# Performance work log

Measured on AMD Instinct MI355X. Metric: run time of the kernel, lower is better.

Reference implementation:

```python
import jax, jax.numpy as jnp
import numpy as np

NH = 12
LEVEL = 4  # Lmin = 2**LEVEL = 16


def _build_sets(T, Lmin):
    l_list, r_list = [], []
    L = Lmin
    while L <= T:
        for i in range(T // L):
            l_list.append(i * L)
            r_list.append((i + 1) * L - 1)
        L *= 2
    return np.asarray(l_list, np.int32), np.asarray(r_list, np.int32)


def _get_slice(x_cum, l_idx, r_idx):
    # x_cum: [B,nh,T,hs]; returns inclusive range-sums x[l..r] via cumsum diffs
    r = x_cum[:, :, r_idx, :]
    l = x_cum[:, :, np.maximum(np.asarray(l_idx) - 1, 0), :]
    mask = (np.asarray(l_idx) >= 1).astype(x_cum.dtype)[None, None, :, None]
    return r - l * mask


def _get_slice_dyn(x_cum, l_idx, r_idx):
    # same but with traced/jnp indices (tail term)
    r = x_cum[:, :, r_idx, :]
    l = x_cum[:, :, jnp.maximum(l_idx - 1, 0), :]
    mask = (l_idx >= 1).astype(x_cum.dtype)[None, None, :, None]
    return r - l * mask


def setup_inputs() -> dict:
    key = jax.random.key(0)
    k0, k1, k2, k3 = jax.random.split(key, 4)
    B, T, C = 8, 2048, 768
    hs = C // NH
    s = 0.02
    return {
        "x": jax.random.normal(k0, (B, T, C), jnp.float32),
        "Wqkv": jax.random.normal(k1, (3 * C, C), jnp.float32) * s,
        "Wproj": jax.random.normal(k2, (C, C), jnp.float32) * s,
        "Wv": jax.random.normal(k3, (hs, hs * hs), jnp.float32) * s,
        "bv": jnp.zeros((hs,), jnp.float32),
    }


def reference(x, Wqkv, Wproj, Wv, bv):
    B, T, C = x.shape
    nh = NH
    hs = C // nh
    Lmin = 2 ** LEVEL
    scale = 1.0 / jnp.sqrt(jnp.asarray(hs, x.dtype))

    qkv = x @ Wqkv.T  # [B,T,3C]
    q, k, v0 = jnp.split(qkv, 3, axis=-1)
    q = q.reshape(B, T, nh, hs).transpose(0, 2, 1, 3)   # [B,nh,T,hs]
    k = k.reshape(B, T, nh, hs).transpose(0, 2, 1, 3)
    v0 = v0.reshape(B, T, nh, hs).transpose(0, 2, 1, 3)

    # v = v_proj(outer(k, v0).flatten)  == einsum with Wv reshaped [hs,hs,hs]
    Wv3 = Wv.reshape(hs, hs, hs)
    v = jnp.einsum('bhti,bhtj,eij->bhte', k, v0, Wv3) + bv

    k_cum = jnp.cumsum(k, axis=2)
    v_cum = jnp.cumsum(v, axis=2)

    l_idx, r_idx = _build_sets(T, Lmin)  # static dyadic sets
    K = _get_slice(k_cum, l_idx, r_idx)  # [B,nh,S,hs]
    V = _get_slice(v_cum, l_idx, r_idx)

    t_idx = jnp.arange(T)
    mask = t_idx[:, None] >= jnp.asarray(r_idx)[None, :]  # [T,S]
    logits = jnp.einsum('bhtd,bhsd->bhts', q, K) * scale
    logits = jnp.where(mask[None, None], logits, -jnp.inf)

    # tail: remainder within the current Lmin block
    l_tail = (t_idx // Lmin) * Lmin
    K_tail = _get_slice_dyn(k_cum, l_tail, t_idx)  # [B,nh,T,hs]
    V_tail = _get_slice_dyn(v_cum, l_tail, t_idx)
    tail_logits = jnp.sum(q * K_tail, axis=-1) * scale  # [B,nh,T]

    att = jax.nn.softmax(jnp.concatenate([logits, tail_logits[..., None]], axis=-1), axis=-1)
    out = jnp.einsum('bhts,bhsd->bhtd', att[..., :-1], V) + att[..., -1:] * V_tail
    out = out.transpose(0, 2, 1, 3).reshape(B, T, C)
    return out @ Wproj.T
```

## Files before the change

kernel.cpp:

```cpp
#include <hip/hip_runtime.h>


typedef float  f32x4  __attribute__((ext_vector_type(4)));
typedef _Float16 half8 __attribute__((ext_vector_type(8)));
typedef _Float16 half4 __attribute__((ext_vector_type(4)));

#define DEV __device__ __forceinline__
#define MFMA16(a, b, c) __builtin_amdgcn_mfma_f32_16x16x32_f16((a), (b), (c), 0, 0, 0)
#define GLOAD16(gp, lp)                                                  \
  __builtin_amdgcn_global_load_lds(                                      \
      (const __attribute__((address_space(1))) unsigned int*)(gp),       \
      (__attribute__((address_space(3))) unsigned int*)(lp), 16, 0, 0)

__global__ __launch_bounds__(256) void k_cast16(const float* __restrict__ in,
                                                _Float16* __restrict__ outh, int n4) {
  int i = blockIdx.x * 256 + threadIdx.x;
  if (i >= n4) return;
  f32x4 v = ((const f32x4*)in)[i];
  half4 o;
#pragma unroll
  for (int c = 0; c < 4; ++c) o[c] = (_Float16)v[c];
  ((half4*)outh)[i] = o;
}

__global__ __launch_bounds__(256, 3) void k_gemm_qkv(
    const _Float16* __restrict__ A16, const _Float16* __restrict__ B16,
    _Float16* __restrict__ qo, _Float16* __restrict__ ko, _Float16* __restrict__ v0o) {
  __shared__ _Float16 sA[128][64], sB[128][64];
  const int K = 768;
  int tid = threadIdx.x, lane = tid & 63, wave = tid >> 6;
  int l15 = lane & 15, g = lane >> 4;
  int wr = wave >> 1, wc = wave & 1;
  int wg = (blockIdx.x & 7) * 288 + (blockIdx.x >> 3);
  int n0 = (wg % 18) * 128, m0 = (wg / 18) * 128;
  f32x4 acc[4][4];
#pragma unroll
  for (int a = 0; a < 4; ++a)
#pragma unroll
    for (int b = 0; b < 4; ++b) acc[a][b] = f32x4{0.f, 0.f, 0.f, 0.f};
  int rsel = lane >> 3;
  int csel = (lane & 7) ^ rsel;
  for (int k0 = 0; k0 < K; k0 += 64) {
#pragma unroll
    for (int r = 0; r < 4; ++r) {
      int row = wave * 32 + r * 8 + rsel;
      GLOAD16(&A16[(size_t)(m0 + row) * K + k0 + csel * 8], &sA[wave * 32 + r * 8][0]);
      GLOAD16(&B16[(size_t)(n0 + row) * K + k0 + csel * 8], &sB[wave * 32 + r * 8][0]);
    }
    __syncthreads();
#pragma unroll
    for (int kk = 0; kk < 2; ++kk) {
      int kc = kk * 4 + g;
      int cc = ((kc ^ (l15 & 7)) << 3);
      half8 af[4], bf[4];
#pragma unroll
      for (int mf = 0; mf < 4; ++mf) af[mf] = *(const half8*)&sA[wr * 64 + mf * 16 + l15][cc];
#pragma unroll
      for (int nf = 0; nf < 4; ++nf) bf[nf] = *(const half8*)&sB[wc * 64 + nf * 16 + l15][cc];
#pragma unroll
      for (int mf = 0; mf < 4; ++mf)
#pragma unroll
        for (int nf = 0; nf < 4; ++nf)
          acc[mf][nf] = MFMA16(af[mf], bf[nf], acc[mf][nf]);
    }
    __syncthreads();
  }
  int sec = n0 / 768;
  int nb = n0 - sec * 768;
#pragma unroll
  for (int mf = 0; mf < 4; ++mf)
#pragma unroll
    for (int nf = 0; nf < 4; ++nf)
#pragma unroll
      for (int r = 0; r < 4; ++r) {
        int m = m0 + wr * 64 + mf * 16 + (g << 2) + r;
        int n = nb + wc * 64 + nf * 16 + l15;
        int b = m >> 11, t = m & 2047;
        int h = n >> 6, d = n & 63;
        size_t idx = (((size_t)b * 12 + h) * 2048 + t) * 64 + d;
        _Float16 val = (_Float16)acc[mf][nf][r];
        if (sec == 0) qo[idx] = val;
        else if (sec == 1) ko[idx] = val;
        else v0o[idx] = val;
      }
}

__global__ __launch_bounds__(256, 3) void k_veins(
    const _Float16* __restrict__ kh, const _Float16* __restrict__ v0g,
    const _Float16* __restrict__ Wvh, const float* __restrict__ bv,
    _Float16* __restrict__ vout) {
  __shared__ _Float16 ks[256][72];
  __shared__ _Float16 sB[2][64][64];
  int tid = threadIdx.x, lane = tid & 63, wave = tid >> 6;
  int l15 = lane & 15, g = lane >> 4, g8 = g << 3;
  size_t row0 = (size_t)blockIdx.x * 256;

  int srow_lo = wave * 8 + (lane >> 3);
  int scsrc = (lane & 7) ^ (lane >> 3);
  auto STAGE = [&](int b, int i) {
#pragma unroll
    for (int h = 0; h < 2; ++h) {
      GLOAD16(&Wvh[(size_t)(h * 32 + srow_lo) * 4096 + i * 64 + (scsrc << 3)],
              ((_Float16*)sB) + (size_t)b * 4096 + (h * 256 + wave * 64) * 8);
    }
  };

#pragma unroll
  for (int r = 0; r < 8; ++r) {
    int row = (tid >> 3) + r * 32;
    int c8 = (tid & 7) << 3;
    *(half8*)&ks[row][c8] = *(const half8*)&kh[(row0 + row) * 64 + c8];
  }
  half8 v0r[4][2];
#pragma unroll
  for (int mf = 0; mf < 4; ++mf) {
    size_t rb = (row0 + wave * 64 + mf * 16 + l15) * 64;
#pragma unroll
    for (int kk = 0; kk < 2; ++kk)
      v0r[mf][kk] = *(const half8*)&v0g[rb + kk * 32 + g8];
  }
  f32x4 acc[4][4];
#pragma unroll
  for (int a = 0; a < 4; ++a)
#pragma unroll
    for (int b = 0; b < 4; ++b) acc[a][b] = f32x4{0.f, 0.f, 0.f, 0.f};

  STAGE(0, 0);
  __syncthreads();
  int r0 = wave * 64 + l15;
  for (int i8 = 0; i8 < 8; ++i8) {
    half8 kr0 = *(const half8*)&ks[r0][i8 * 8];
    half8 kr1 = *(const half8*)&ks[r0 + 16][i8 * 8];
    half8 kr2 = *(const half8*)&ks[r0 + 32][i8 * 8];
    half8 kr3 = *(const half8*)&ks[r0 + 48][i8 * 8];
#pragma unroll
    for (int ii = 0; ii < 8; ++ii) {
      int i = i8 * 8 + ii;
      int cur = i & 1;
      if (i < 63) STAGE(cur ^ 1, i + 1);
      half8 b0[4], b1[4];
#pragma unroll
      for (int nf = 0; nf < 4; ++nf) {
        b0[nf] = *(const half8*)&sB[cur][nf * 16 + l15][((g ^ (l15 & 7)) << 3)];
        b1[nf] = *(const half8*)&sB[cur][nf * 16 + l15][(((4 + g) ^ (l15 & 7)) << 3)];
      }
      _Float16 kv0 = kr0[ii], kv1 = kr1[ii], kv2 = kr2[ii], kv3 = kr3[ii];
      {
        half8 a0 = v0r[0][0] * kv0, a1 = v0r[1][0] * kv1;
        half8 a2 = v0r[2][0] * kv2, a3 = v0r[3][0] * kv3;
#pragma unroll
        for (int nf = 0; nf < 4; ++nf) {
          acc[0][nf] = MFMA16(a0, b0[nf], acc[0][nf]);
          acc[1][nf] = MFMA16(a1, b0[nf], acc[1][nf]);
          acc[2][nf] = MFMA16(a2, b0[nf], acc[2][nf]);
          acc[3][nf] = MFMA16(a3, b0[nf], acc[3][nf]);
        }
      }
      {
        half8 a0 = v0r[0][1] * kv0, a1 = v0r[1][1] * kv1;
        half8 a2 = v0r[2][1] * kv2, a3 = v0r[3][1] * kv3;
#pragma unroll
        for (int nf = 0; nf < 4; ++nf) {
          acc[0][nf] = MFMA16(a0, b1[nf], acc[0][nf]);
          acc[1][nf] = MFMA16(a1, b1[nf], acc[1][nf]);
          acc[2][nf] = MFMA16(a2, b1[nf], acc[2][nf]);
          acc[3][nf] = MFMA16(a3, b1[nf], acc[3][nf]);
        }
      }
      __syncthreads();
    }
  }
#pragma unroll
  for (int mf = 0; mf < 4; ++mf)
#pragma unroll
    for (int nf = 0; nf < 4; ++nf) {
      int e = (nf << 4) + l15;
      float bve = bv[e];
#pragma unroll
      for (int r = 0; r < 4; ++r) {
        int row = wave * 64 + mf * 16 + (g << 2) + r;
        vout[(row0 + row) * 64 + e] = (_Float16)(acc[mf][nf][r] + bve);
      }
    }
}

__global__ __launch_bounds__(256) void k_segments(
    const _Float16* __restrict__ kmat, const _Float16* __restrict__ vmat,
    _Float16* __restrict__ Ks, _Float16* __restrict__ Vt) {
  __shared__ float Ls[255][64];
  int bh = blockIdx.x, tid = threadIdx.x;
  size_t bh2048 = (size_t)bh * 2048;
  for (int task = tid; task < 8192; task += 256) {
    int seg = task >> 6, d = task & 63;
    const _Float16* p = kmat + (bh2048 + seg * 16) * 64 + d;
    float s = 0.f;
#pragma unroll
    for (int u = 0; u < 16; ++u) s += (float)p[u * 64];
    Ls[seg][d] = s;
  }
  __syncthreads();
  {
    int bprev = 0, bcur = 128, cnt = 64;
    for (int lev = 1; lev < 8; ++lev) {
      for (int task = tid; task < cnt * 64; task += 256) {
        int i = task >> 6, d = task & 63;
        Ls[bcur + i][d] = Ls[bprev + 2 * i][d] + Ls[bprev + 2 * i + 1][d];
      }
      __syncthreads();
      bprev = bcur; bcur += cnt; cnt >>= 1;
    }
  }
  for (int task = tid; task < 16384; task += 256) {
    int seg = task >> 6;
    float v = (seg < 255) ? Ls[seg][task & 63] : 0.f;
    Ks[(size_t)bh * 16384 + task] = (_Float16)v;
  }
  __syncthreads();
  for (int task = tid; task < 8192; task += 256) {
    int seg = task >> 6, d = task & 63;
    const _Float16* p = vmat + (bh2048 + seg * 16) * 64 + d;
    float s = 0.f;
#pragma unroll
    for (int u = 0; u < 16; ++u) s += (float)p[u * 64];
    Ls[seg][d] = s;
  }
  __syncthreads();
  {
    int bprev = 0, bcur = 128, cnt = 64;
    for (int lev = 1; lev < 8; ++lev) {
      for (int task = tid; task < cnt * 64; task += 256) {
        int i = task >> 6, d = task & 63;
        Ls[bcur + i][d] = Ls[bprev + 2 * i][d] + Ls[bprev + 2 * i + 1][d];
      }
      __syncthreads();
      bprev = bcur; bcur += cnt; cnt >>= 1;
    }
  }
  for (int task = tid; task < 16384; task += 256) {
    int d = task >> 8, seg = task & 255;
    float v = (seg < 255) ? Ls[seg][d] : 0.f;
    Vt[(size_t)bh * 16384 + task] = (_Float16)v;
  }
}

__global__ __launch_bounds__(256) void k_tails(
    const _Float16* __restrict__ km, const _Float16* __restrict__ vm,
    _Float16* __restrict__ tKg, _Float16* __restrict__ tVt) {
  int bh = blockIdx.x >> 3, seg16 = (blockIdx.x & 7) * 16;
  int wave = threadIdx.x >> 6, lane = threadIdx.x & 63;
  for (int task = wave; task < 32; task += 4) {
    int blk = seg16 + (task >> 1);
    size_t base = ((size_t)bh * 2048 + blk * 16) * 64 + lane;
    if (!(task & 1)) {
      float ka = 0.f;
      _Float16* o = tKg + (((size_t)bh * 128 + blk) * 16) * 64 + lane;
#pragma unroll
      for (int t = 0; t < 16; ++t) {
        ka += (float)km[base + t * 64];
        o[t * 64] = (_Float16)ka;
      }
    } else {
      float va = 0.f;
      half8 lo = {}, hi = {};
#pragma unroll
      for (int t = 0; t < 8; ++t) {
        va += (float)vm[base + t * 64];
        lo[t] = (_Float16)va;
      }
#pragma unroll
      for (int t = 0; t < 8; ++t) {
        va += (float)vm[base + (t + 8) * 64];
        hi[t] = (_Float16)va;
      }
      _Float16* o = tVt + (((size_t)bh * 128 + blk) * 64 + lane) * 16;
      ((half8*)o)[0] = lo;
      ((half8*)o)[1] = hi;
    }
  }
}

__global__ __launch_bounds__(256, 3) void k_attn2(
    const _Float16* __restrict__ qm,
    const _Float16* __restrict__ tKg, const _Float16* __restrict__ tVt,
    const _Float16* __restrict__ Ks, const _Float16* __restrict__ Vt,
    _Float16* __restrict__ outp) {
  __shared__ __align__(16) _Float16 P[4][16][280];
  int tid = threadIdx.x, lane = tid & 63, wave = tid >> 6;
  int orig = blockIdx.y * 32 + blockIdx.x;
  int wg = (orig & 7) * 384 + (orig >> 3);
  int tile = wg & 31, bh = wg >> 5;
  int t0 = tile * 64, tw0 = t0 + wave * 16;
  int blkw = tile * 4 + wave;
  size_t bh2048 = (size_t)bh * 2048;
  int l15 = lane & 15, g = lane >> 4, g8 = g << 3;

  half8 qf0, qf1;
  {
    const _Float16* qp = qm + (bh2048 + tw0 + l15) * 64 + g8;
    qf0 = *(const half8*)qp;
    qf1 = *(const half8*)(qp + 32);
  }
  half8 t0f, t1f;
  {
    const _Float16* tp = tKg + (((size_t)bh * 128 + blkw) * 16 + l15) * 64 + g8;
    t0f = *(const half8*)tp;
    t1f = *(const half8*)(tp + 32);
  }
  unsigned mA = 0, mE = 0;
#pragma unroll
  for (int nf = 0; nf < 16; ++nf) {
    int seg = nf * 16 + l15;
    if (seg < 255) {
      int m = 256 - seg;
      int cl = 32 - __clz(m - 1);
      int lev = 8 - cl;
      int rdx = (seg - (256 - (256 >> lev)) + 1) * (16 << lev) - 1;
      if (rdx < tw0) mA |= 1u << nf;
      else if (rdx == tw0 + 15) mE |= 1u << nf;
    }
  }

  const _Float16* KsB = Ks + (size_t)bh * 16384;
  const _Float16* VB = Vt + (size_t)bh * 16384;
  f32x4 acc[17];
#pragma unroll
  for (int i = 0; i < 17; ++i) acc[i] = f32x4{0.f, 0.f, 0.f, 0.f};

#define LOADKS(dst, ks_)                                                 \
  {                                                                      \
    const _Float16* ph = KsB + (size_t)((ks_) * 32 + l15) * 64 + g8;     \
    (dst)[0] = *(const half8*)ph;                                        \
    (dst)[1] = *(const half8*)(ph + 32);                                 \
    (dst)[2] = *(const half8*)(ph + 1024);                               \
    (dst)[3] = *(const half8*)(ph + 1056);                               \
  }
#define QKMFMA(src, ks_)                                                 \
  {                                                                      \
    acc[2 * (ks_)]     = MFMA16(qf0, (src)[0], acc[2 * (ks_)]);          \
    acc[2 * (ks_)]     = MFMA16(qf1, (src)[1], acc[2 * (ks_)]);          \
    acc[2 * (ks_) + 1] = MFMA16(qf0, (src)[2], acc[2 * (ks_) + 1]);      \
    acc[2 * (ks_) + 1] = MFMA16(qf1, (src)[3], acc[2 * (ks_) + 1]);      \
  }

  half8 fr[3][4];
  LOADKS(fr[0], 0);
  LOADKS(fr[1], 1);
  __builtin_amdgcn_s_setprio(1);
#pragma unroll
  for (int ks = 0; ks < 8; ++ks) {
    if (ks < 6) LOADKS(fr[(ks + 2) % 3], ks + 2);
    QKMFMA(fr[ks % 3], ks);
  }
  acc[16] = MFMA16(qf0, t0f, acc[16]);
  acc[16] = MFMA16(qf1, t1f, acc[16]);
  __builtin_amdgcn_s_setprio(0);

  const float c = 0.125f * 1.44269504f;
  float mx[4], sm[4], et[4];
#pragma unroll
  for (int r = 0; r < 4; ++r) {
    int tr = g * 4 + r;
    mx[r] = (l15 == tr) ? acc[16][r] * c : -3.0e38f;
  }
#pragma unroll
  for (int nf = 0; nf < 16; ++nf) {
    bool bA = (mA >> nf) & 1, bE = (mE >> nf) & 1;
#pragma unroll
    for (int r = 0; r < 4; ++r) {
      bool u = bA || (bE && g == 3 && r == 3);
      if (u) mx[r] = fmaxf(mx[r], acc[nf][r] * c);
    }
  }
#pragma unroll
  for (int off = 1; off < 16; off <<= 1)
#pragma unroll
    for (int r = 0; r < 4; ++r) mx[r] = fmaxf(mx[r], __shfl_xor(mx[r], off));
#pragma unroll
  for (int r = 0; r < 4; ++r) {
    int tr = g * 4 + r;
    et[r] = (l15 == tr) ? exp2f(acc[16][r] * c - mx[r]) : 0.f;
    sm[r] = et[r];
  }
#pragma unroll
  for (int nf = 0; nf < 16; ++nf) {
    bool bA = (mA >> nf) & 1, bE = (mE >> nf) & 1;
#pragma unroll
    for (int r = 0; r < 4; ++r) {
      bool u = bA || (bE && g == 3 && r == 3);
      float e = u ? exp2f(acc[nf][r] * c - mx[r]) : 0.f;
      acc[nf][r] = e;
      sm[r] += e;
    }
  }
#pragma unroll
  for (int off = 1; off < 16; off <<= 1)
#pragma unroll
    for (int r = 0; r < 4; ++r) sm[r] += __shfl_xor(sm[r], off);
  float inv[4];
#pragma unroll
  for (int r = 0; r < 4; ++r) inv[r] = 1.f / sm[r];

#define LOADVT(dst, ks_)                                                 \
  {                                                                      \
    const _Float16* pv = VB + (size_t)l15 * 256 + (ks_) * 32 + g8;       \
    (dst)[0] = *(const half8*)pv;                                        \
    (dst)[1] = *(const half8*)(pv + 16 * 256);                           \
    (dst)[2] = *(const half8*)(pv + 32 * 256);                           \
    (dst)[3] = *(const half8*)(pv + 48 * 256);                           \
  }

  half8 vr[3][4];
  LOADVT(vr[0], 0);
  LOADVT(vr[1], 1);

  {
    half4 z4 = {};
    *(half4*)&P[wave][lane >> 2][256 + (lane & 3) * 4] = z4;
  }
#pragma unroll
  for (int nf = 0; nf < 16; ++nf)
#pragma unroll
    for (int r = 0; r < 4; ++r)
      P[wave][g * 4 + r][nf * 16 + l15] = (_Float16)acc[nf][r];
#pragma unroll
  for (int r = 0; r < 4; ++r)
    if (l15 == g * 4 + r) P[wave][l15][256 + l15] = (_Float16)et[r];

  f32x4 oa[4];
#pragma unroll
  for (int i = 0; i < 4; ++i) oa[i] = f32x4{0.f, 0.f, 0.f, 0.f};
  __builtin_amdgcn_s_setprio(1);
#pragma unroll
  for (int ks = 0; ks < 8; ++ks) {
    if (ks < 6) LOADVT(vr[(ks + 2) % 3], ks + 2);
    half8 pa = *(const half8*)&P[wave][l15][ks * 32 + g8];
#pragma unroll
    for (int n2 = 0; n2 < 4; ++n2)
      oa[n2] = MFMA16(pa, vr[ks % 3][n2], oa[n2]);
  }
  {
    half8 pa = *(const half8*)&P[wave][l15][256 + (g & 1) * 8];
    const _Float16* tvb = tVt + ((size_t)bh * 128 + blkw) * 1024;
#pragma unroll
    for (int n2 = 0; n2 < 4; ++n2) {
      half8 vt = {};
      if (g < 2)
        vt = *(const half8*)(tvb + (size_t)(n2 * 16 + l15) * 16 + g8);
      oa[n2] = MFMA16(pa, vt, oa[n2]);
    }
  }
  __builtin_amdgcn_s_setprio(0);
#undef LOADKS
#undef QKMFMA
#undef LOADVT
  int b = bh / 12, h = bh - b * 12;
  size_t obase = ((size_t)b * 2048 + tw0) * 768 + h * 64;
#pragma unroll
  for (int n2 = 0; n2 < 4; ++n2)
#pragma unroll
    for (int r = 0; r < 4; ++r)
      outp[obase + (size_t)(g * 4 + r) * 768 + n2 * 16 + l15] = (_Float16)(oa[n2][r] * inv[r]);
}

__global__ __launch_bounds__(256, 3) void k_gemm_proj(
    const _Float16* __restrict__ A16, const _Float16* __restrict__ B16,
    float* __restrict__ C) {
  __shared__ _Float16 sA[128][64], sB[128][64];
  const int K = 768;
  int tid = threadIdx.x, lane = tid & 63, wave = tid >> 6;
  int l15 = lane & 15, g = lane >> 4;
  int wr = wave >> 1, wc = wave & 1;
  int wg = (blockIdx.x & 7) * 96 + (blockIdx.x >> 3);
  int n0 = (wg % 6) * 128, m0 = (wg / 6) * 128;
  f32x4 acc[4][4];
#pragma unroll
  for (int a = 0; a < 4; ++a)
#pragma unroll
    for (int b = 0; b < 4; ++b) acc[a][b] = f32x4{0.f, 0.f, 0.f, 0.f};
  int rsel = lane >> 3;
  int csel = (lane & 7) ^ rsel;
  for (int k0 = 0; k0 < K; k0 += 64) {
#pragma unroll
    for (int r = 0; r < 4; ++r) {
      int row = wave * 32 + r * 8 + rsel;
      GLOAD16(&A16[(size_t)(m0 + row) * K + k0 + csel * 8], &sA[wave * 32 + r * 8][0]);
      GLOAD16(&B16[(size_t)(n0 + row) * K + k0 + csel * 8], &sB[wave * 32 + r * 8][0]);
    }
    __syncthreads();
#pragma unroll
    for (int kk = 0; kk < 2; ++kk) {
      int kc = kk * 4 + g;
      int cc = ((kc ^ (l15 & 7)) << 3);
      half8 af[4], bf[4];
#pragma unroll
      for (int mf = 0; mf < 4; ++mf) af[mf] = *(const half8*)&sA[wr * 64 + mf * 16 + l15][cc];
#pragma unroll
      for (int nf = 0; nf < 4; ++nf) bf[nf] = *(const half8*)&sB[wc * 64 + nf * 16 + l15][cc];
#pragma unroll
      for (int mf = 0; mf < 4; ++mf)
#pragma unroll
        for (int nf = 0; nf < 4; ++nf)
          acc[mf][nf] = MFMA16(af[mf], bf[nf], acc[mf][nf]);
    }
    __syncthreads();
  }
#pragma unroll
  for (int mf = 0; mf < 4; ++mf)
#pragma unroll
    for (int nf = 0; nf < 4; ++nf)
#pragma unroll
      for (int r = 0; r < 4; ++r) {
        int m = m0 + wr * 64 + mf * 16 + (g << 2) + r;
        int n = n0 + wc * 64 + nf * 16 + l15;
        C[(size_t)m * 768 + n] = acc[mf][nf][r];
      }
}

extern "C" void kernel_launch(void* const* d_in, const int* in_sizes, int n_in,
                              void* d_out, int out_size, void* d_ws, size_t ws_size,
                              hipStream_t stream) {
  const float* x = (const float*)d_in[0];
  const float* Wqkv = (const float*)d_in[1];
  const float* Wproj = (const float*)d_in[2];
  const float* Wv = (const float*)d_in[3];
  const float* bv = (const float*)d_in[4];
  float* out = (float*)d_out;
  char* ws = (char*)d_ws;
  size_t off = 0;
  auto alloc = [&](size_t bytes) -> void* {
    void* p = (void*)(ws + off);
    off += (bytes + 255) & ~(size_t)255;
    return p;
  };
  _Float16* x16  = (_Float16*)alloc(12582912ull * 2);
  _Float16* wq16 = (_Float16*)alloc(1769472ull * 2);
  _Float16* wv16 = (_Float16*)alloc(262144ull * 2 + 8192);
  _Float16* wp16 = (_Float16*)alloc(589824ull * 2);
  _Float16* q16  = (_Float16*)alloc(12582912ull * 2);
  _Float16* k16  = (_Float16*)alloc(12582912ull * 2);
  _Float16* v016 = (_Float16*)alloc(12582912ull * 2);
  _Float16* vm16 = (_Float16*)alloc(12582912ull * 2);
  _Float16* Ks   = (_Float16*)alloc(1572864ull * 2);
  _Float16* Vt   = (_Float16*)alloc(1572864ull * 2);
  _Float16* tKg  = (_Float16*)alloc(12582912ull * 2);
  _Float16* tVt  = (_Float16*)alloc(12582912ull * 2);
  _Float16* outp = (_Float16*)alloc(12582912ull * 2);

  k_cast16<<<dim3(12288), dim3(256), 0, stream>>>(x, x16, 3145728);
  k_cast16<<<dim3(1728), dim3(256), 0, stream>>>(Wqkv, wq16, 442368);
  k_cast16<<<dim3(256), dim3(256), 0, stream>>>(Wv, wv16, 65536);
  k_cast16<<<dim3(576), dim3(256), 0, stream>>>(Wproj, wp16, 147456);
  k_gemm_qkv<<<dim3(2304), dim3(256), 0, stream>>>(x16, wq16, q16, k16, v016);
  k_veins<<<dim3(768), dim3(256), 0, stream>>>(k16, v016, wv16, bv, vm16);
  k_segments<<<dim3(96), dim3(256), 0, stream>>>(k16, vm16, Ks, Vt);
  k_tails<<<dim3(768), dim3(256), 0, stream>>>(k16, vm16, tKg, tVt);
  k_attn2<<<dim3(32, 96), dim3(256), 0, stream>>>(q16, tKg, tVt, Ks, Vt, outp);
  k_gemm_proj<<<dim3(768), dim3(256), 0, stream>>>(outp, wp16, out);
}
```

Measured before the change: 364.1 us.

## Stage K and V chunks through shared LDS with double-buffered direct loads

In the attention kernel, each wave used to load the whole per-head K and V tiles from global memory into registers on its own, even though all four waves in a block read the same data. The new code stages 32-row K chunks and 32-column V chunks into double-buffered LDS with global_load_lds, using an XOR swizzle to avoid bank conflicts, so each chunk is fetched once per block. This cuts redundant global/L2 traffic and frees registers. In exchange it adds a block-wide barrier per chunk, about 16KB more LDS next to the P buffer, and drops the s_setprio hints.

```diff
diff --git a/kernel.cpp b/kernel.cpp
--- a/kernel.cpp
+++ b/kernel.cpp
@@ -285,6 +285,8 @@
     const _Float16* __restrict__ Ks, const _Float16* __restrict__ Vt,
     _Float16* __restrict__ outp) {
   __shared__ __align__(16) _Float16 P[4][16][280];
+  __shared__ __align__(16) _Float16 sKs[2][32][64];
+  __shared__ __align__(16) _Float16 sVt[2][64][32];
   int tid = threadIdx.x, lane = tid & 63, wave = tid >> 6;
   int orig = blockIdx.y * 32 + blockIdx.x;
   int wg = (orig & 7) * 384 + (orig >> 3);
@@ -294,18 +296,31 @@
   size_t bh2048 = (size_t)bh * 2048;
   int l15 = lane & 15, g = lane >> 4, g8 = g << 3;
 
-  half8 qf0, qf1;
+  const _Float16* KsB = Ks + (size_t)bh * 16384;
+  const _Float16* VB = Vt + (size_t)bh * 16384;
+
+  auto STAGE_K = [&](int buf, int c) {
+    GLOAD16(KsB + (size_t)(c * 32 + wave * 8 + (lane >> 3)) * 64 +
+                (((lane & 7) ^ ((lane >> 3) & 7)) << 3),
+            &sKs[buf][wave * 8][0]);
+  };
+  auto STAGE_VT = [&](int buf, int c) {
+    GLOAD16(VB + (size_t)(wave * 16 + (lane >> 2)) * 256 + c * 32 +
+                (((lane & 3) ^ ((lane >> 2) & 3)) << 3),
+            &sVt[buf][wave * 16][0]);
+  };
+
+  half8 qf0, qf1, t0f, t1f;
   {
     const _Float16* qp = qm + (bh2048 + tw0 + l15) * 64 + g8;
     qf0 = *(const half8*)qp;
     qf1 = *(const half8*)(qp + 32);
-  }
-  half8 t0f, t1f;
-  {
     const _Float16* tp = tKg + (((size_t)bh * 128 + blkw) * 16 + l15) * 64 + g8;
     t0f = *(const half8*)tp;
     t1f = *(const half8*)(tp + 32);
   }
+  STAGE_K(0, 0);
+
   unsigned mA = 0, mE = 0;
 #pragma unroll
   for (int nf = 0; nf < 16; ++nf) {
@@ -320,47 +335,37 @@
     }
   }
 
-  const _Float16* KsB = Ks + (size_t)bh * 16384;
-  const _Float16* VB = Vt + (size_t)bh * 16384;
   f32x4 acc[17];
 #pragma unroll
   for (int i = 0; i < 17; ++i) acc[i] = f32x4{0.f, 0.f, 0.f, 0.f};
 
-#define LOADKS(dst, ks_)                                                 \
-  {                                                                      \
-    const _Float16* ph = KsB + (size_t)((ks_) * 32 + l15) * 64 + g8;     \
-    (dst)[0] = *(const half8*)ph;                                        \
-    (dst)[1] = *(const half8*)(ph + 32);                                 \
-    (dst)[2] = *(const half8*)(ph + 1024);                               \
-    (dst)[3] = *(const half8*)(ph + 1056);                               \
-  }
-#define QKMFMA(src, ks_)                                                 \
-  {                                                                      \
-    acc[2 * (ks_)]     = MFMA16(qf0, (src)[0], acc[2 * (ks_)]);          \
-    acc[2 * (ks_)]     = MFMA16(qf1, (src)[1], acc[2 * (ks_)]);          \
-    acc[2 * (ks_) + 1] = MFMA16(qf0, (src)[2], acc[2 * (ks_) + 1]);      \
-    acc[2 * (ks_) + 1] = MFMA16(qf1, (src)[3], acc[2 * (ks_) + 1]);      \
-  }
-
-  half8 fr[3][4];
-  LOADKS(fr[0], 0);
-  LOADKS(fr[1], 1);
-  __builtin_amdgcn_s_setprio(1);
-#pragma unroll
-  for (int ks = 0; ks < 8; ++ks) {
-    if (ks < 6) LOADKS(fr[(ks + 2) % 3], ks + 2);
-    QKMFMA(fr[ks % 3], ks);
+  __syncthreads();
+#pragma unroll
+  for (int c = 0; c < 8; ++c) {
+    if (c < 7) STAGE_K((c + 1) & 1, c + 1);
+    int bs = c & 1;
+#pragma unroll
+    for (int p = 0; p < 2; ++p) {
+      int row = p * 16 + l15;
+      half8 b0 = *(const half8*)&sKs[bs][row][(g ^ (l15 & 7)) << 3];
+      half8 b1 = *(const half8*)&sKs[bs][row][((g + 4) ^ (l15 & 7)) << 3];
+      acc[2 * c + p] = MFMA16(qf0, b0, acc[2 * c + p]);
+      acc[2 * c + p] = MFMA16(qf1, b1, acc[2 * c + p]);
+    }
+    __syncthreads();
   }
   acc[16] = MFMA16(qf0, t0f, acc[16]);
   acc[16] = MFMA16(qf1, t1f, acc[16]);
-  __builtin_amdgcn_s_setprio(0);
-
-  const float c = 0.125f * 1.44269504f;
+
+  STAGE_VT(0, 0);
+  STAGE_VT(1, 1);
+
+  const float c2 = 0.125f * 1.44269504f;
   float mx[4], sm[4], et[4];
 #pragma unroll
   for (int r = 0; r < 4; ++r) {
     int tr = g * 4 + r;
-    mx[r] = (l15 == tr) ? acc[16][r] * c : -3.0e38f;
+    mx[r] = (l15 == tr) ? acc[16][r] * c2 : -3.0e38f;
   }
 #pragma unroll
   for (int nf = 0; nf < 16; ++nf) {
@@ -368,7 +373,7 @@
 #pragma unroll
     for (int r = 0; r < 4; ++r) {
       bool u = bA || (bE && g == 3 && r == 3);
-      if (u) mx[r] = fmaxf(mx[r], acc[nf][r] * c);
+      if (u) mx[r] = fmaxf(mx[r], acc[nf][r] * c2);
     }
   }
 #pragma unroll
@@ -378,7 +383,7 @@
 #pragma unroll
   for (int r = 0; r < 4; ++r) {
     int tr = g * 4 + r;
-    et[r] = (l15 == tr) ? exp2f(acc[16][r] * c - mx[r]) : 0.f;
+    et[r] = (l15 == tr) ? exp2f(acc[16][r] * c2 - mx[r]) : 0.f;
     sm[r] = et[r];
   }
 #pragma unroll
@@ -387,7 +392,7 @@
 #pragma unroll
     for (int r = 0; r < 4; ++r) {
       bool u = bA || (bE && g == 3 && r == 3);
-      float e = u ? exp2f(acc[nf][r] * c - mx[r]) : 0.f;
+      float e = u ? exp2f(acc[nf][r] * c2 - mx[r]) : 0.f;
       acc[nf][r] = e;
       sm[r] += e;
     }
@@ -399,19 +404,6 @@
   float inv[4];
 #pragma unroll
   for (int r = 0; r < 4; ++r) inv[r] = 1.f / sm[r];
-
-#define LOADVT(dst, ks_)                                                 \
-  {                                                                      \
-    const _Float16* pv = VB + (size_t)l15 * 256 + (ks_) * 32 + g8;       \
-    (dst)[0] = *(const half8*)pv;                                        \
-    (dst)[1] = *(const half8*)(pv + 16 * 256);                           \
-    (dst)[2] = *(const half8*)(pv + 32 * 256);                           \
-    (dst)[3] = *(const half8*)(pv + 48 * 256);                           \
-  }
-
-  half8 vr[3][4];
-  LOADVT(vr[0], 0);
-  LOADVT(vr[1], 1);
 
   {
     half4 z4 = {};
@@ -429,14 +421,18 @@
   f32x4 oa[4];
 #pragma unroll
   for (int i = 0; i < 4; ++i) oa[i] = f32x4{0.f, 0.f, 0.f, 0.f};
-  __builtin_amdgcn_s_setprio(1);
-#pragma unroll
-  for (int ks = 0; ks < 8; ++ks) {
-    if (ks < 6) LOADVT(vr[(ks + 2) % 3], ks + 2);
-    half8 pa = *(const half8*)&P[wave][l15][ks * 32 + g8];
-#pragma unroll
-    for (int n2 = 0; n2 < 4; ++n2)
-      oa[n2] = MFMA16(pa, vr[ks % 3][n2], oa[n2]);
+  __syncthreads();
+#pragma unroll
+  for (int c = 0; c < 8; ++c) {
+    int bs = c & 1;
+    half8 pa = *(const half8*)&P[wave][l15][c * 32 + g8];
+#pragma unroll
+    for (int n2 = 0; n2 < 4; ++n2) {
+      half8 vb = *(const half8*)&sVt[bs][n2 * 16 + l15][(g ^ (l15 & 3)) << 3];
+      oa[n2] = MFMA16(pa, vb, oa[n2]);
+    }
+    __syncthreads();
+    if (c < 6) STAGE_VT(bs, c + 2);
   }
   {
     half8 pa = *(const half8*)&P[wave][l15][256 + (g & 1) * 8];
@@ -449,10 +445,6 @@
       oa[n2] = MFMA16(pa, vt, oa[n2]);
     }
   }
-  __builtin_amdgcn_s_setprio(0);
-#undef LOADKS
-#undef QKMFMA
-#undef LOADVT
   int b = bh / 12, h = bh - b * 12;
   size_t obase = ((size_t)b * 2048 + tw0) * 768 + h * 64;
 #pragma unroll
```

New measurement: 312.1 us. -14.3%, faster.
